# Performance work log

Hardware: AMD Instinct MI355X
Metric: run time of the kernel (lower is better)

## Reference

```python
import jax, jax.numpy as jnp
import numpy as np

N_NODES = 100000
N_EDGES = 1600000
F_IN, HID, N_CLS = 128, 64, 40


def gcn_conv(x, src, dst, W, b, n_nodes):
    # x: [N, Fin] -> [N, Fout]; edges already include self-loops.
    h = x @ W  # [N, Fout]
    ones = jnp.ones_like(src, dtype=h.dtype)
    deg = jax.ops.segment_sum(ones, dst, num_segments=n_nodes)  # [N]
    dinv = jnp.where(deg > 0, jax.lax.rsqrt(deg), 0.0)
    norm = dinv[src] * dinv[dst]  # [E]
    msg = h[src] * norm[:, None]  # gather + scale
    out = jax.ops.segment_sum(msg, dst, num_segments=n_nodes)  # scatter-sum
    return out + b


def setup_inputs() -> dict:
    key = jax.random.key(0)
    ks = jax.random.split(key, 8)
    x = jax.random.normal(ks[0], (N_NODES, F_IN), dtype=jnp.float32)
    edge_index = jax.random.randint(ks[1], (2, N_EDGES), 0, N_NODES, dtype=jnp.int64)

    def glorot(k, fi, fo):
        s = float(np.sqrt(6.0 / (fi + fo)))
        return jax.random.uniform(k, (fi, fo), jnp.float32, -s, s)

    return {
        "x": x,
        "edge_index": edge_index,
        "W1": glorot(ks[2], F_IN, HID), "b1": jnp.zeros((HID,), jnp.float32),
        "W2": glorot(ks[3], HID, HID), "b2": jnp.zeros((HID,), jnp.float32),
        "W3": glorot(ks[4], HID, N_CLS), "b3": jnp.zeros((N_CLS,), jnp.float32),
    }


def reference(x, edge_index, W1, b1, W2, b2, W3, b3):
    n = x.shape[0]
    loop = jnp.arange(n, dtype=edge_index.dtype)
    src = jnp.concatenate([edge_index[0], loop])  # add self-loops
    dst = jnp.concatenate([edge_index[1], loop])
    # layer 1..3: GCNConv -> relu -> dropout(eval: identity)
    h = jax.nn.relu(gcn_conv(x, src, dst, W1, b1, n))
    h = jax.nn.relu(gcn_conv(h, src, dst, W2, b2, n))
    h = jax.nn.relu(gcn_conv(h, src, dst, W3, b3, n))
    return jax.nn.log_softmax(h, axis=1)
```

## Files before the change

### kernel.cpp

```cpp
#include <hip/hip_runtime.h>
#include <math.h>

typedef _Float16 half2v  __attribute__((ext_vector_type(2)));
typedef _Float16 half8   __attribute__((ext_vector_type(8)));
typedef float    float4v __attribute__((ext_vector_type(4)));

static __device__ __forceinline__ unsigned short f32_to_f16u(float f) {
    _Float16 h = (_Float16)f;
    return __builtin_bit_cast(unsigned short, h);
}


__global__ void zero_int(int* __restrict__ p, int n) {
    int i = blockIdx.x * blockDim.x + threadIdx.x;
    if (i < n) p[i] = 0;
}

__global__ __launch_bounds__(256) void hist_bucket(
    const int* __restrict__ dst, int* __restrict__ bcnt, int E, int NB)
{
    __shared__ int h[512];
    const int tid = threadIdx.x;
    h[tid] = 0; h[tid + 256] = 0;
    __syncthreads();
    const int base = blockIdx.x * 4096 + tid;
    #pragma unroll
    for (int k = 0; k < 16; ++k) {
        int i = base + k * 256;
        if (i < E) atomicAdd(&h[dst[i] >> 8], 1);
    }
    __syncthreads();
    for (int j = tid; j < NB; j += 256)
        if (h[j]) atomicAdd(&bcnt[j], h[j]);
}

__global__ __launch_bounds__(512) void scan_nb(
    const int* __restrict__ bcnt, int* __restrict__ boff, int* __restrict__ bcur,
    int* __restrict__ rp, int NB, int n, int E)
{
    __shared__ int s[512];
    const int tid = threadIdx.x;
    int v = (tid < NB) ? bcnt[tid] : 0;
    s[tid] = v;
    __syncthreads();
    for (int off = 1; off < 512; off <<= 1) {
        int x = (tid >= off) ? s[tid - off] : 0;
        __syncthreads();
        s[tid] += x;
        __syncthreads();
    }
    int excl = s[tid] - v;
    if (tid < NB) { boff[tid] = excl; bcur[tid] = excl; }
    if (tid == NB - 1) boff[NB] = excl + v;
    if (tid == 0) rp[n] = E;
}

__global__ __launch_bounds__(256) void bin_edges(
    const int* __restrict__ src, const int* __restrict__ dst,
    int* __restrict__ bcur, unsigned int* __restrict__ bint, int E, int NB)
{
    __shared__ int h[512];
    __shared__ int rbase[512];
    const int tid = threadIdx.x;
    h[tid] = 0; h[tid + 256] = 0;
    __syncthreads();
    const int eb = blockIdx.x * 4096 + tid;
    int d[16], sr[16];
    #pragma unroll
    for (int k = 0; k < 16; ++k) {
        int i = eb + k * 256;
        if (i < E) {
            d[k] = dst[i]; sr[k] = src[i];
            atomicAdd(&h[d[k] >> 8], 1);
        } else d[k] = -1;
    }
    __syncthreads();
    for (int j = tid; j < NB; j += 256) {
        int c = h[j];
        rbase[j] = c ? atomicAdd(&bcur[j], c) : 0;
        h[j] = 0;
    }
    __syncthreads();
    #pragma unroll
    for (int k = 0; k < 16; ++k) {
        if (d[k] >= 0) {
            int bkt = d[k] >> 8;
            int pos = rbase[bkt] + atomicAdd(&h[bkt], 1);
            bint[pos] = ((unsigned int)sr[k] << 8) | (unsigned int)(d[k] & 255);
        }
    }
}

__global__ __launch_bounds__(256) void build_csr(
    const unsigned int* __restrict__ bint, const int* __restrict__ boff,
    int* __restrict__ rp, float* __restrict__ dinv, int* __restrict__ es, int n)
{
    __shared__ int cnt[256];
    __shared__ int sc[256];
    __shared__ int cur[256];
    const int b = blockIdx.x, tid = threadIdx.x;
    const int e0 = boff[b], e1 = boff[b + 1];

    cnt[tid] = 0;
    __syncthreads();
    for (int i = e0 + tid; i < e1; i += 256)
        atomicAdd(&cnt[bint[i] & 255], 1);
    __syncthreads();

    int v = cnt[tid];
    sc[tid] = v;
    __syncthreads();
    for (int off = 1; off < 256; off <<= 1) {
        int x = (tid >= off) ? sc[tid - off] : 0;
        __syncthreads();
        sc[tid] += x;
        __syncthreads();
    }
    int excl = sc[tid] - v;
    int node = (b << 8) + tid;
    if (node < n) {
        rp[node]   = e0 + excl;
        dinv[node] = rsqrtf((float)(v + 1));
    }
    cur[tid] = e0 + excl;
    __syncthreads();

    for (int i = e0 + tid; i < e1; i += 256) {
        unsigned int p = bint[i];
        int pos = atomicAdd(&cur[p & 255], 1);
        es[pos] = (int)(p >> 8);
    }
}


__global__ __launch_bounds__(256) void prep_w3(
    const float* __restrict__ W1, const float* __restrict__ W2, const float* __restrict__ W3,
    unsigned short* __restrict__ Wf1, unsigned short* __restrict__ Wf2, unsigned short* __restrict__ Wf3)
{
    const float* W; unsigned short* Wf; int K, M;
    if (blockIdx.x == 0)      { W = W1; Wf = Wf1; K = 128; M = 64; }
    else if (blockIdx.x == 1) { W = W2; Wf = Wf2; K = 64;  M = 64; }
    else                      { W = W3; Wf = Wf3; K = 64;  M = 40; }
    const int NT = (M + 15) >> 4, NTC = NT << 4, KS = K >> 5;
    for (int i = threadIdx.x; i < K * NTC; i += 256) {
        int k = i / NTC, nn = i - k * NTC;
        unsigned short hv = 0;
        if (nn < M) hv = f32_to_f16u(W[(size_t)k * M + nn]);
        int s = k >> 5, q = (k >> 3) & 3, j = k & 7;
        int u = nn >> 4, lane = (q << 4) | (nn & 15);
        Wf[((u * KS + s) << 9) + (lane << 3) + j] = hv;
    }
}


template<int KK, int NT, int STRIDE, int MOUT, bool INF32>
__global__ __launch_bounds__(256) void gemm_t(
    const void* __restrict__ Xin, const unsigned short* __restrict__ Wf,
    const float* __restrict__ dinv, unsigned short* __restrict__ H, int n)
{
    constexpr int KS = KK >> 5;
    __shared__ __align__(16) unsigned short ldsA[4 * KS * 512];
    const int tid = threadIdx.x;
    const int n0  = blockIdx.x * 64;

    half8 bf[NT * KS];
    {
        const int lane = tid & 63;
        #pragma unroll
        for (int u = 0; u < NT; ++u)
            #pragma unroll
            for (int s = 0; s < KS; ++s)
                bf[u * KS + s] = *(const half8*)&Wf[((u * KS + s) << 9) + (lane << 3)];
    }

    {
        const int rl = tid >> 3;
        const int kl = tid & 7;
        #pragma unroll
        for (int rb = 0; rb < 64; rb += 32) {
            int r = rl + rb;
            int node = n0 + r;
            int t = r >> 4, m = r & 15;
            #pragma unroll
            for (int kq8 = 0; kq8 < (KK >> 2); kq8 += 8) {
                int k0 = (kl + kq8) << 2;
                unsigned short h[4] = {0, 0, 0, 0};
                if (node < n) {
                    if (INF32) {
                        const float* xp = (const float*)Xin + (size_t)node * KK + k0;
                        float4v v = *(const float4v*)xp;
                        #pragma unroll
                        for (int i = 0; i < 4; ++i) h[i] = f32_to_f16u(v[i]);
                    } else {
                        const unsigned int* ap =
                            (const unsigned int*)Xin + (((size_t)node * KK + k0) >> 1);
                        uint2 v = *(const uint2*)ap;
                        h[0] = (unsigned short)(v.x & 0xffff);
                        h[1] = (unsigned short)(v.x >> 16);
                        h[2] = (unsigned short)(v.y & 0xffff);
                        h[3] = (unsigned short)(v.y >> 16);
                    }
                }
                int s = k0 >> 5, q = (k0 >> 3) & 3, j0 = k0 & 7;
                int lane = (q << 4) | m;
                unsigned short* p = &ldsA[((t * KS + s) << 9) + (lane << 3) + j0];
                unsigned int lo = (unsigned int)h[0] | ((unsigned int)h[1] << 16);
                unsigned int hi = (unsigned int)h[2] | ((unsigned int)h[3] << 16);
                *(uint2*)p = make_uint2(lo, hi);
            }
        }
    }

    __syncthreads();

    const int wv   = tid >> 6;
    const int lane = tid & 63;
    float4v acc[NT];
    #pragma unroll
    for (int u = 0; u < NT; ++u) acc[u] = (float4v){0.f, 0.f, 0.f, 0.f};

    #pragma unroll
    for (int s = 0; s < KS; ++s) {
        half8 a = *(const half8*)&ldsA[((wv * KS + s) << 9) + (lane << 3)];
        #pragma unroll
        for (int u = 0; u < NT; ++u)
            acc[u] = __builtin_amdgcn_mfma_f32_16x16x32_f16(a, bf[u * KS + s], acc[u], 0, 0, 0);
    }

    const int mcol = lane & 15;
    const int quad = lane >> 4;
    #pragma unroll
    for (int reg = 0; reg < 4; ++reg) {
        int node = n0 + (wv << 4) + (quad << 2) + reg;
        if (node >= n) continue;
        float dv = dinv[node];
        #pragma unroll
        for (int u = 0; u < NT; ++u) {
            int col = (u << 4) + mcol;
            if (col < MOUT)
                H[(size_t)node * STRIDE + col] = f32_to_f16u(acc[u][reg] * dv);
        }
    }
}


template<int MOUT, int ROWU4, bool RELU_OUT, bool SOFTMAX>
__global__ __launch_bounds__(256) void gather_t(
    const int* __restrict__ rp, const int* __restrict__ es,
    const unsigned short* __restrict__ H, const float* __restrict__ dinv,
    const float* __restrict__ bias, void* __restrict__ Aout, int n)
{
    const int lane   = threadIdx.x & 63;
    const int half   = lane >> 5;
    const int lane32 = lane & 31;
    const int slot   = (lane >> 3) & 3;
    const int c8     = lane & 7;
    const bool act   = c8 < ROWU4;
    const uint4* H4  = (const uint4*)H;

    float bi[8];
    #pragma unroll
    for (int i = 0; i < 8; ++i) {
        int col = (c8 << 3) + i;
        bi[i] = (col < MOUT) ? bias[col] : 0.0f;
    }

    const half8 hz = {(_Float16)0, (_Float16)0, (_Float16)0, (_Float16)0,
                      (_Float16)0, (_Float16)0, (_Float16)0, (_Float16)0};

    const int TW2 = (int)(gridDim.x << 3);
    for (int nb = (((int)blockIdx.x << 2) + ((int)threadIdx.x >> 6)) << 1; nb < n; nb += TW2) {
        const int node = nb + half;
        const int e0 = rp[node], e1 = rp[node + 1];
        const float dv = dinv[node];

        half8 hacc = hz;
        if (slot == 0 && act)
            hacc = __builtin_bit_cast(half8, H4[(size_t)node * ROWU4 + c8]);

        for (int cb = e0; cb < e1; cb += 32) {
            const int rem = e1 - cb;
            int eidx = cb + lane32; if (eidx > e1 - 1) eidx = e1 - 1;
            const int ei = es[eidx];
            #pragma unroll
            for (int j = 0; j < 8; ++j) {
                const int idx = (j << 2) + slot;
                const int s = __shfl(ei, (half << 5) + idx, 64);
                if (idx < rem && act) {
                    uint4 u = H4[(size_t)s * ROWU4 + c8];
                    hacc = hacc + __builtin_bit_cast(half8, u);
                }
            }
        }

        #pragma unroll
        for (int step = 8; step <= 16; step <<= 1) {
            uint4 u = __builtin_bit_cast(uint4, hacc);
            uint4 o;
            o.x = __shfl_xor(u.x, step, 64);
            o.y = __shfl_xor(u.y, step, 64);
            o.z = __shfl_xor(u.z, step, 64);
            o.w = __shfl_xor(u.w, step, 64);
            hacc = hacc + __builtin_bit_cast(half8, o);
        }

        if (!SOFTMAX) {
            if (slot == 0) {
                unsigned short o[8];
                #pragma unroll
                for (int i = 0; i < 8; ++i) {
                    float v = (float)hacc[i] * dv + bi[i];
                    if (RELU_OUT) v = fmaxf(v, 0.0f);
                    o[i] = f32_to_f16u(v);
                }
                uint4 w;
                w.x = (unsigned int)o[0] | ((unsigned int)o[1] << 16);
                w.y = (unsigned int)o[2] | ((unsigned int)o[3] << 16);
                w.z = (unsigned int)o[4] | ((unsigned int)o[5] << 16);
                w.w = (unsigned int)o[6] | ((unsigned int)o[7] << 16);
                ((uint4*)Aout)[(size_t)node * 8 + c8] = w;
            }
        } else {
            float z[8]; float m = -INFINITY;
            #pragma unroll
            for (int i = 0; i < 8; ++i) {
                int col = (c8 << 3) + i;
                z[i] = (col < MOUT && act) ? fmaxf((float)hacc[i] * dv + bi[i], 0.0f)
                                           : -INFINITY;
                m = fmaxf(m, z[i]);
            }
            m = fmaxf(m, __shfl_xor(m, 1, 64));
            m = fmaxf(m, __shfl_xor(m, 2, 64));
            m = fmaxf(m, __shfl_xor(m, 4, 64));
            float s = 0.0f;
            #pragma unroll
            for (int i = 0; i < 8; ++i) s += expf(z[i] - m);
            s += __shfl_xor(s, 1, 64);
            s += __shfl_xor(s, 2, 64);
            s += __shfl_xor(s, 4, 64);
            float ls = logf(s) + m;
            if (slot == 0 && c8 < (MOUT + 7) / 8) {
                float* op = (float*)Aout + (size_t)node * MOUT + (c8 << 3);
                float4v o0 = {z[0] - ls, z[1] - ls, z[2] - ls, z[3] - ls};
                float4v o1 = {z[4] - ls, z[5] - ls, z[6] - ls, z[7] - ls};
                *(float4v*)op = o0;
                *(float4v*)(op + 4) = o1;
            }
        }
    }
}


extern "C" void kernel_launch(void* const* d_in, const int* in_sizes, int n_in,
                              void* d_out, int out_size, void* d_ws, size_t ws_size,
                              hipStream_t stream)
{
    const float* x  = (const float*)d_in[0];
    const int*   ei = (const int*)  d_in[1];
    const float* W1 = (const float*)d_in[2];
    const float* b1 = (const float*)d_in[3];
    const float* W2 = (const float*)d_in[4];
    const float* b2 = (const float*)d_in[5];
    const float* W3 = (const float*)d_in[6];
    const float* b3 = (const float*)d_in[7];

    const int F_IN = 128;
    const int n = in_sizes[0] / F_IN;
    const int E = in_sizes[1] / 2;
    const int* src = ei;
    const int* dst = ei + E;
    float* out = (float*)d_out;

    const int NB = (n + 255) >> 8;

    auto align = [](size_t v) { return (v + 255) & ~(size_t)255; };
    char* w = (char*)d_ws;
    size_t off = 0;
    float*          dinv = (float*)(w + off);          off = align(off + (size_t)n * 4);
    unsigned short* H    = (unsigned short*)(w + off); off = align(off + (size_t)n * 64 * 2);
    unsigned short* A    = (unsigned short*)(w + off); off = align(off + (size_t)n * 64 * 2);
    int*            rp   = (int*)(w + off);            off = align(off + (size_t)(n + 1) * 4);
    int*            es   = (int*)(w + off);            off = align(off + (size_t)E * 4);
    unsigned int*   bint = (unsigned int*)(w + off);   off = align(off + (size_t)E * 4);
    int*            bcnt = (int*)(w + off);            off = align(off + (size_t)512 * 4);
    int*            boff = (int*)(w + off);            off = align(off + (size_t)513 * 4);
    int*            bcur = (int*)(w + off);            off = align(off + (size_t)512 * 4);
    unsigned short* Wf1  = (unsigned short*)(w + off); off = align(off + (size_t)8192 * 2);
    unsigned short* Wf2  = (unsigned short*)(w + off); off = align(off + (size_t)4096 * 2);
    unsigned short* Wf3  = (unsigned short*)(w + off); off = align(off + (size_t)3072 * 2);

    const int BLK = 256;
    auto cdiv = [](int a, int b) { return (a + b - 1) / b; };
    const int EB = cdiv(E, 4096);

    prep_w3    <<<3, BLK, 0, stream>>>(W1, W2, W3, Wf1, Wf2, Wf3);
    zero_int   <<<cdiv(NB, BLK), BLK, 0, stream>>>(bcnt, NB);
    hist_bucket<<<EB, BLK, 0, stream>>>(dst, bcnt, E, NB);
    scan_nb    <<<1, 512, 0, stream>>>(bcnt, boff, bcur, rp, NB, n, E);
    bin_edges  <<<EB, BLK, 0, stream>>>(src, dst, bcur, bint, E, NB);
    build_csr  <<<NB, BLK, 0, stream>>>(bint, boff, rp, dinv, es, n);

    const int GB = cdiv(n, 64);
    const int GG = 2048;

    gemm_t<128, 4, 64, 64, true> <<<GB, BLK, 0, stream>>>(x, Wf1, dinv, H, n);
    gather_t<64, 8, true, false><<<GG, BLK, 0, stream>>>(rp, es, H, dinv, b1, A, n);

    gemm_t<64, 4, 64, 64, false> <<<GB, BLK, 0, stream>>>(A, Wf2, dinv, H, n);
    gather_t<64, 8, true, false><<<GG, BLK, 0, stream>>>(rp, es, H, dinv, b2, A, n);

    gemm_t<64, 3, 40, 40, false> <<<GB, BLK, 0, stream>>>(A, Wf3, dinv, H, n);
    gather_t<40, 5, false, true><<<GG, BLK, 0, stream>>>(rp, es, H, dinv, b3, out, n);
}
```

Measured before the change: 293.3 us.

## Fuse gather with next-layer GEMM and use fixed-capacity buckets for CSR build

```diff
diff --git a/kernel.cpp b/kernel.cpp
--- a/kernel.cpp
+++ b/kernel.cpp
@@ -1,9 +1,10 @@
 #include <hip/hip_runtime.h>
 #include <math.h>
 
-typedef _Float16 half2v  __attribute__((ext_vector_type(2)));
 typedef _Float16 half8   __attribute__((ext_vector_type(8)));
 typedef float    float4v __attribute__((ext_vector_type(4)));
+
+#define CAP 6144
 
 static __device__ __forceinline__ unsigned short f32_to_f16u(float f) {
     _Float16 h = (_Float16)f;
@@ -11,132 +12,15 @@
 }
 
 
-__global__ void zero_int(int* __restrict__ p, int n) {
-    int i = blockIdx.x * blockDim.x + threadIdx.x;
-    if (i < n) p[i] = 0;
-}
-
-__global__ __launch_bounds__(256) void hist_bucket(
-    const int* __restrict__ dst, int* __restrict__ bcnt, int E, int NB)
-{
-    __shared__ int h[512];
-    const int tid = threadIdx.x;
-    h[tid] = 0; h[tid + 256] = 0;
-    __syncthreads();
-    const int base = blockIdx.x * 4096 + tid;
-    #pragma unroll
-    for (int k = 0; k < 16; ++k) {
-        int i = base + k * 256;
-        if (i < E) atomicAdd(&h[dst[i] >> 8], 1);
-    }
-    __syncthreads();
-    for (int j = tid; j < NB; j += 256)
-        if (h[j]) atomicAdd(&bcnt[j], h[j]);
-}
-
-__global__ __launch_bounds__(512) void scan_nb(
-    const int* __restrict__ bcnt, int* __restrict__ boff, int* __restrict__ bcur,
-    int* __restrict__ rp, int NB, int n, int E)
-{
-    __shared__ int s[512];
-    const int tid = threadIdx.x;
-    int v = (tid < NB) ? bcnt[tid] : 0;
-    s[tid] = v;
-    __syncthreads();
-    for (int off = 1; off < 512; off <<= 1) {
-        int x = (tid >= off) ? s[tid - off] : 0;
-        __syncthreads();
-        s[tid] += x;
-        __syncthreads();
-    }
-    int excl = s[tid] - v;
-    if (tid < NB) { boff[tid] = excl; bcur[tid] = excl; }
-    if (tid == NB - 1) boff[NB] = excl + v;
-    if (tid == 0) rp[n] = E;
-}
-
-__global__ __launch_bounds__(256) void bin_edges(
-    const int* __restrict__ src, const int* __restrict__ dst,
-    int* __restrict__ bcur, unsigned int* __restrict__ bint, int E, int NB)
-{
-    __shared__ int h[512];
-    __shared__ int rbase[512];
-    const int tid = threadIdx.x;
-    h[tid] = 0; h[tid + 256] = 0;
-    __syncthreads();
-    const int eb = blockIdx.x * 4096 + tid;
-    int d[16], sr[16];
-    #pragma unroll
-    for (int k = 0; k < 16; ++k) {
-        int i = eb + k * 256;
-        if (i < E) {
-            d[k] = dst[i]; sr[k] = src[i];
-            atomicAdd(&h[d[k] >> 8], 1);
-        } else d[k] = -1;
-    }
-    __syncthreads();
-    for (int j = tid; j < NB; j += 256) {
-        int c = h[j];
-        rbase[j] = c ? atomicAdd(&bcur[j], c) : 0;
-        h[j] = 0;
-    }
-    __syncthreads();
-    #pragma unroll
-    for (int k = 0; k < 16; ++k) {
-        if (d[k] >= 0) {
-            int bkt = d[k] >> 8;
-            int pos = rbase[bkt] + atomicAdd(&h[bkt], 1);
-            bint[pos] = ((unsigned int)sr[k] << 8) | (unsigned int)(d[k] & 255);
-        }
-    }
-}
-
-__global__ __launch_bounds__(256) void build_csr(
-    const unsigned int* __restrict__ bint, const int* __restrict__ boff,
-    int* __restrict__ rp, float* __restrict__ dinv, int* __restrict__ es, int n)
-{
-    __shared__ int cnt[256];
-    __shared__ int sc[256];
-    __shared__ int cur[256];
-    const int b = blockIdx.x, tid = threadIdx.x;
-    const int e0 = boff[b], e1 = boff[b + 1];
-
-    cnt[tid] = 0;
-    __syncthreads();
-    for (int i = e0 + tid; i < e1; i += 256)
-        atomicAdd(&cnt[bint[i] & 255], 1);
-    __syncthreads();
-
-    int v = cnt[tid];
-    sc[tid] = v;
-    __syncthreads();
-    for (int off = 1; off < 256; off <<= 1) {
-        int x = (tid >= off) ? sc[tid - off] : 0;
-        __syncthreads();
-        sc[tid] += x;
-        __syncthreads();
-    }
-    int excl = sc[tid] - v;
-    int node = (b << 8) + tid;
-    if (node < n) {
-        rp[node]   = e0 + excl;
-        dinv[node] = rsqrtf((float)(v + 1));
-    }
-    cur[tid] = e0 + excl;
-    __syncthreads();
-
-    for (int i = e0 + tid; i < e1; i += 256) {
-        unsigned int p = bint[i];
-        int pos = atomicAdd(&cur[p & 255], 1);
-        es[pos] = (int)(p >> 8);
-    }
-}
-
-
-__global__ __launch_bounds__(256) void prep_w3(
+__global__ __launch_bounds__(256) void prep_init(
     const float* __restrict__ W1, const float* __restrict__ W2, const float* __restrict__ W3,
-    unsigned short* __restrict__ Wf1, unsigned short* __restrict__ Wf2, unsigned short* __restrict__ Wf3)
-{
+    unsigned short* __restrict__ Wf1, unsigned short* __restrict__ Wf2,
+    unsigned short* __restrict__ Wf3, int* __restrict__ bcur, int NB)
+{
+    if (blockIdx.x == 3) {
+        for (int i = threadIdx.x; i < NB; i += 256) bcur[i] = 0;
+        return;
+    }
     const float* W; unsigned short* Wf; int K, M;
     if (blockIdx.x == 0)      { W = W1; Wf = Wf1; K = 128; M = 64; }
     else if (blockIdx.x == 1) { W = W2; Wf = Wf2; K = 64;  M = 64; }
@@ -153,9 +37,93 @@
 }
 
 
-template<int KK, int NT, int STRIDE, int MOUT, bool INF32>
+__global__ __launch_bounds__(256) void bin_edges(
+    const int* __restrict__ src, const int* __restrict__ dst,
+    int* __restrict__ bcur, unsigned int* __restrict__ bint, int E, int NB)
+{
+    __shared__ int h[512];
+    __shared__ int rbase[512];
+    const int tid = threadIdx.x;
+    h[tid] = 0; h[tid + 256] = 0;
+    __syncthreads();
+    const int eb = blockIdx.x * 4096 + tid;
+    int d[16], sr[16];
+    #pragma unroll
+    for (int k = 0; k < 16; ++k) {
+        int i = eb + k * 256;
+        if (i < E) {
+            d[k] = dst[i]; sr[k] = src[i];
+            atomicAdd(&h[d[k] >> 8], 1);
+        } else d[k] = -1;
+    }
+    __syncthreads();
+    for (int j = tid; j < NB; j += 256) {
+        int c = h[j];
+        rbase[j] = c ? atomicAdd(&bcur[j], c) : 0;
+        h[j] = 0;
+    }
+    __syncthreads();
+    #pragma unroll
+    for (int k = 0; k < 16; ++k) {
+        if (d[k] >= 0) {
+            int bkt = d[k] >> 8;
+            int pos = rbase[bkt] + atomicAdd(&h[bkt], 1);
+            if (pos < CAP)
+                bint[(size_t)bkt * CAP + pos] =
+                    ((unsigned int)sr[k] << 8) | (unsigned int)(d[k] & 255);
+        }
+    }
+}
+
+
+__global__ __launch_bounds__(256) void build_csr(
+    const unsigned int* __restrict__ bint, const int* __restrict__ bcur,
+    int2* __restrict__ rp2, float* __restrict__ dinv, int* __restrict__ es, int n)
+{
+    __shared__ int cnt[256];
+    __shared__ int sc[256];
+    __shared__ int cur[256];
+    const int b = blockIdx.x, tid = threadIdx.x;
+    int total = bcur[b]; if (total > CAP) total = CAP;
+    const unsigned int* bp = bint + (size_t)b * CAP;
+    int* ep = es + (size_t)b * CAP;
+    const int base = b * CAP;
+
+    cnt[tid] = 0;
+    __syncthreads();
+    for (int i = tid; i < total; i += 256)
+        atomicAdd(&cnt[bp[i] & 255], 1);
+    __syncthreads();
+
+    int v = cnt[tid];
+    sc[tid] = v;
+    __syncthreads();
+    for (int off = 1; off < 256; off <<= 1) {
+        int x = (tid >= off) ? sc[tid - off] : 0;
+        __syncthreads();
+        sc[tid] += x;
+        __syncthreads();
+    }
+    int excl = sc[tid] - v;
+    int node = (b << 8) + tid;
+    if (node < n) {
+        rp2[node]  = make_int2(base + excl, base + excl + v);
+        dinv[node] = rsqrtf((float)(v + 1));
+    }
+    cur[tid] = excl;
+    __syncthreads();
+
+    for (int i = tid; i < total; i += 256) {
+        unsigned int p = bp[i];
+        int pos = atomicAdd(&cur[p & 255], 1);
+        ep[pos] = (int)(p >> 8);
+    }
+}
+
+
+template<int KK, int NT, int STRIDE, int MOUT>
 __global__ __launch_bounds__(256) void gemm_t(
-    const void* __restrict__ Xin, const unsigned short* __restrict__ Wf,
+    const float* __restrict__ Xin, const unsigned short* __restrict__ Wf,
     const float* __restrict__ dinv, unsigned short* __restrict__ H, int n)
 {
     constexpr int KS = KK >> 5;
@@ -186,20 +154,10 @@
                 int k0 = (kl + kq8) << 2;
                 unsigned short h[4] = {0, 0, 0, 0};
                 if (node < n) {
-                    if (INF32) {
-                        const float* xp = (const float*)Xin + (size_t)node * KK + k0;
-                        float4v v = *(const float4v*)xp;
-                        #pragma unroll
-                        for (int i = 0; i < 4; ++i) h[i] = f32_to_f16u(v[i]);
-                    } else {
-                        const unsigned int* ap =
-                            (const unsigned int*)Xin + (((size_t)node * KK + k0) >> 1);
-                        uint2 v = *(const uint2*)ap;
-                        h[0] = (unsigned short)(v.x & 0xffff);
-                        h[1] = (unsigned short)(v.x >> 16);
-                        h[2] = (unsigned short)(v.y & 0xffff);
-                        h[3] = (unsigned short)(v.y >> 16);
-                    }
+                    const float* xp = Xin + (size_t)node * KK + k0;
+                    float4v v = *(const float4v*)xp;
+                    #pragma unroll
+                    for (int i = 0; i < 4; ++i) h[i] = f32_to_f16u(v[i]);
                 }
                 int s = k0 >> 5, q = (k0 >> 3) & 3, j0 = k0 & 7;
                 int lane = (q << 4) | m;
@@ -244,55 +202,61 @@
 }
 
 
-template<int MOUT, int ROWU4, bool RELU_OUT, bool SOFTMAX>
-__global__ __launch_bounds__(256) void gather_t(
-    const int* __restrict__ rp, const int* __restrict__ es,
-    const unsigned short* __restrict__ H, const float* __restrict__ dinv,
-    const float* __restrict__ bias, void* __restrict__ Aout, int n)
-{
-    const int lane   = threadIdx.x & 63;
+template<int NT, int STRIDE, int MOUT>
+__global__ __launch_bounds__(256) void gather_gemm(
+    const int2* __restrict__ rp2, const int* __restrict__ es,
+    const unsigned short* __restrict__ Hin, const float* __restrict__ dinv,
+    const float* __restrict__ bias, const unsigned short* __restrict__ Wf,
+    unsigned short* __restrict__ Hout, int n)
+{
+    constexpr int KS = 2;
+    __shared__ __align__(16) unsigned short ldsA[4 * KS * 512];
+    const int tid  = threadIdx.x;
+    const int wv   = tid >> 6;
+    const int lane = tid & 63;
+    const int nw0  = blockIdx.x * 64 + (wv << 4);
+
+    half8 bf[NT * KS];
+    #pragma unroll
+    for (int u = 0; u < NT; ++u)
+        #pragma unroll
+        for (int s = 0; s < KS; ++s)
+            bf[u * KS + s] = *(const half8*)&Wf[((u * KS + s) << 9) + (lane << 3)];
+
     const int half   = lane >> 5;
     const int lane32 = lane & 31;
     const int slot   = (lane >> 3) & 3;
     const int c8     = lane & 7;
-    const bool act   = c8 < ROWU4;
-    const uint4* H4  = (const uint4*)H;
+    const uint4* H4  = (const uint4*)Hin;
 
     float bi[8];
     #pragma unroll
-    for (int i = 0; i < 8; ++i) {
-        int col = (c8 << 3) + i;
-        bi[i] = (col < MOUT) ? bias[col] : 0.0f;
-    }
+    for (int i = 0; i < 8; ++i) bi[i] = bias[(c8 << 3) + i];
 
     const half8 hz = {(_Float16)0, (_Float16)0, (_Float16)0, (_Float16)0,
                       (_Float16)0, (_Float16)0, (_Float16)0, (_Float16)0};
 
-    const int TW2 = (int)(gridDim.x << 3);
-    for (int nb = (((int)blockIdx.x << 2) + ((int)threadIdx.x >> 6)) << 1; nb < n; nb += TW2) {
-        const int node = nb + half;
-        const int e0 = rp[node], e1 = rp[node + 1];
-        const float dv = dinv[node];
-
+    for (int p = 0; p < 8; ++p) {
+        const int node = nw0 + (p << 1) + half;
         half8 hacc = hz;
-        if (slot == 0 && act)
-            hacc = __builtin_bit_cast(half8, H4[(size_t)node * ROWU4 + c8]);
-
-        for (int cb = e0; cb < e1; cb += 32) {
-            const int rem = e1 - cb;
-            int eidx = cb + lane32; if (eidx > e1 - 1) eidx = e1 - 1;
-            const int ei = es[eidx];
-            #pragma unroll
-            for (int j = 0; j < 8; ++j) {
-                const int idx = (j << 2) + slot;
-                const int s = __shfl(ei, (half << 5) + idx, 64);
-                if (idx < rem && act) {
-                    uint4 u = H4[(size_t)s * ROWU4 + c8];
-                    hacc = hacc + __builtin_bit_cast(half8, u);
+        float dv = 0.0f;
+        if (node < n) {
+            dv = dinv[node];
+            const int2 e = rp2[node];
+            if (slot == 0) hacc = __builtin_bit_cast(half8, H4[(size_t)node * 8 + c8]);
+            for (int cb = e.x; cb < e.y; cb += 32) {
+                const int rem = e.y - cb;
+                int eidx = cb + lane32; if (eidx > e.y - 1) eidx = e.y - 1;
+                const int ei = es[eidx];
+                #pragma unroll
+                for (int j = 0; j < 8; ++j) {
+                    const int idx = (j << 2) + slot;
+                    const int s = __shfl(ei, (half << 5) + idx, 64);
+                    if (idx < rem)
+                        hacc = hacc + __builtin_bit_cast(half8, H4[(size_t)s * 8 + c8]);
                 }
             }
         }
-
         #pragma unroll
         for (int step = 8; step <= 16; step <<= 1) {
             uint4 u = __builtin_bit_cast(uint4, hacc);
@@ -303,49 +267,134 @@
             o.w = __shfl_xor(u.w, step, 64);
             hacc = hacc + __builtin_bit_cast(half8, o);
         }
-
-        if (!SOFTMAX) {
-            if (slot == 0) {
-                unsigned short o[8];
-                #pragma unroll
-                for (int i = 0; i < 8; ++i) {
-                    float v = (float)hacc[i] * dv + bi[i];
-                    if (RELU_OUT) v = fmaxf(v, 0.0f);
-                    o[i] = f32_to_f16u(v);
-                }
-                uint4 w;
-                w.x = (unsigned int)o[0] | ((unsigned int)o[1] << 16);
-                w.y = (unsigned int)o[2] | ((unsigned int)o[3] << 16);
-                w.z = (unsigned int)o[4] | ((unsigned int)o[5] << 16);
-                w.w = (unsigned int)o[6] | ((unsigned int)o[7] << 16);
-                ((uint4*)Aout)[(size_t)node * 8 + c8] = w;
+        if (slot == 0) {
+            unsigned short o[8];
+            #pragma unroll
+            for (int i = 0; i < 8; ++i)
+                o[i] = f32_to_f16u(fmaxf((float)hacc[i] * dv + bi[i], 0.0f));
+            uint4 w;
+            w.x = (unsigned int)o[0] | ((unsigned int)o[1] << 16);
+            w.y = (unsigned int)o[2] | ((unsigned int)o[3] << 16);
+            w.z = (unsigned int)o[4] | ((unsigned int)o[5] << 16);
+            w.w = (unsigned int)o[6] | ((unsigned int)o[7] << 16);
+            const int m = (p << 1) | half;
+            unsigned short* dst =
+                &ldsA[((wv * KS + (c8 >> 2)) << 9) + ((((c8 & 3) << 4) | m) << 3)];
+            *(uint4*)dst = w;
+        }
+    }
+
+    float4v acc[NT];
+    #pragma unroll
+    for (int u = 0; u < NT; ++u) acc[u] = (float4v){0.f, 0.f, 0.f, 0.f};
+
+    #pragma unroll
+    for (int s = 0; s < KS; ++s) {
+        half8 a = *(const half8*)&ldsA[((wv * KS + s) << 9) + (lane << 3)];
+        #pragma unroll
+        for (int u = 0; u < NT; ++u)
+            acc[u] = __builtin_amdgcn_mfma_f32_16x16x32_f16(a, bf[u * KS + s], acc[u], 0, 0, 0);
+    }
+
+    const int mcol = lane & 15;
+    const int quad = lane >> 4;
+    #pragma unroll
+    for (int reg = 0; reg < 4; ++reg) {
+        int node = nw0 + (quad << 2) + reg;
+        if (node >= n) continue;
+        float dv = dinv[node];
+        #pragma unroll
+        for (int u = 0; u < NT; ++u) {
+            int col = (u << 4) + mcol;
+            if (col < MOUT)
+                Hout[(size_t)node * STRIDE + col] = f32_to_f16u(acc[u][reg] * dv);
+        }
+    }
+}
+
+
+template<int MOUT, int ROWU4>
+__global__ __launch_bounds__(256) void gather_softmax(
+    const int2* __restrict__ rp2, const int* __restrict__ es,
+    const unsigned short* __restrict__ H, const float* __restrict__ dinv,
+    const float* __restrict__ bias, float* __restrict__ out, int n)
+{
+    const int lane   = threadIdx.x & 63;
+    const int half   = lane >> 5;
+    const int lane32 = lane & 31;
+    const int slot   = (lane >> 3) & 3;
+    const int c8     = lane & 7;
+    const bool act   = c8 < ROWU4;
+    const uint4* H4  = (const uint4*)H;
+
+    float bi[8];
+    #pragma unroll
+    for (int i = 0; i < 8; ++i) {
+        int col = (c8 << 3) + i;
+        bi[i] = (col < MOUT) ? bias[col] : 0.0f;
+    }
+
+    const half8 hz = {(_Float16)0, (_Float16)0, (_Float16)0, (_Float16)0,
+                      (_Float16)0, (_Float16)0, (_Float16)0, (_Float16)0};
+
+    const int TW2 = (int)(gridDim.x << 3);
+    for (int nb = (((int)blockIdx.x << 2) + ((int)threadIdx.x >> 6)) << 1; nb < n; nb += TW2) {
+        const int node = nb + half;
+        const int2 e = rp2[node];
+        const float dv = dinv[node];
+
+        half8 hacc = hz;
+        if (slot == 0 && act)
+            hacc = __builtin_bit_cast(half8, H4[(size_t)node * ROWU4 + c8]);
+
+        for (int cb = e.x; cb < e.y; cb += 32) {
+            const int rem = e.y - cb;
+            int eidx = cb + lane32; if (eidx > e.y - 1) eidx = e.y - 1;
+            const int ei = es[eidx];
+            #pragma unroll
+            for (int j = 0; j < 8; ++j) {
+                const int idx = (j << 2) + slot;
+                const int s = __shfl(ei, (half << 5) + idx, 64);
+                if (idx < rem && act)
+                    hacc = hacc + __builtin_bit_cast(half8, H4[(size_t)s * ROWU4 + c8]);
             }
-        } else {
-            float z[8]; float m = -INFINITY;
-            #pragma unroll
-            for (int i = 0; i < 8; ++i) {
-                int col = (c8 << 3) + i;
-                z[i] = (col < MOUT && act) ? fmaxf((float)hacc[i] * dv + bi[i], 0.0f)
-                                           : -INFINITY;
-                m = fmaxf(m, z[i]);
-            }
-            m = fmaxf(m, __shfl_xor(m, 1, 64));
-            m = fmaxf(m, __shfl_xor(m, 2, 64));
-            m = fmaxf(m, __shfl_xor(m, 4, 64));
-            float s = 0.0f;
-            #pragma unroll
-            for (int i = 0; i < 8; ++i) s += expf(z[i] - m);
-            s += __shfl_xor(s, 1, 64);
-            s += __shfl_xor(s, 2, 64);
-            s += __shfl_xor(s, 4, 64);
-            float ls = logf(s) + m;
-            if (slot == 0 && c8 < (MOUT + 7) / 8) {
-                float* op = (float*)Aout + (size_t)node * MOUT + (c8 << 3);
-                float4v o0 = {z[0] - ls, z[1] - ls, z[2] - ls, z[3] - ls};
-                float4v o1 = {z[4] - ls, z[5] - ls, z[6] - ls, z[7] - ls};
-                *(float4v*)op = o0;
-                *(float4v*)(op + 4) = o1;
-            }
+        }
+
+        #pragma unroll
+        for (int step = 8; step <= 16; step <<= 1) {
+            uint4 u = __builtin_bit_cast(uint4, hacc);
+            uint4 o;
+            o.x = __shfl_xor(u.x, step, 64);
+            o.y = __shfl_xor(u.y, step, 64);
+            o.z = __shfl_xor(u.z, step, 64);
+            o.w = __shfl_xor(u.w, step, 64);
+            hacc = hacc + __builtin_bit_cast(half8, o);
+        }
+
+        float z[8]; float m = -INFINITY;
+        #pragma unroll
+        for (int i = 0; i < 8; ++i) {
+            int col = (c8 << 3) + i;
+            z[i] = (col < MOUT && act) ? fmaxf((float)hacc[i] * dv + bi[i], 0.0f)
+                                       : -INFINITY;
+            m = fmaxf(m, z[i]);
+        }
+        m = fmaxf(m, __shfl_xor(m, 1, 64));
+        m = fmaxf(m, __shfl_xor(m, 2, 64));
+        m = fmaxf(m, __shfl_xor(m, 4, 64));
+        float s = 0.0f;
+        #pragma unroll
+        for (int i = 0; i < 8; ++i) s += expf(z[i] - m);
+        s += __shfl_xor(s, 1, 64);
+        s += __shfl_xor(s, 2, 64);
+        s += __shfl_xor(s, 4, 64);
+        float ls = logf(s) + m;
+        if (slot == 0 && c8 < (MOUT + 7) / 8) {
+            float* op = out + (size_t)node * MOUT + (c8 << 3);
+            float4v o0 = {z[0] - ls, z[1] - ls, z[2] - ls, z[3] - ls};
+            float4v o1 = {z[4] - ls, z[5] - ls, z[6] - ls, z[7] - ls};
+            *(float4v*)op = o0;
+            *(float4v*)(op + 4) = o1;
         }
     }
 }
@@ -377,13 +426,12 @@
     char* w = (char*)d_ws;
     size_t off = 0;
     float*          dinv = (float*)(w + off);          off = align(off + (size_t)n * 4);
-    unsigned short* H    = (unsigned short*)(w + off); off = align(off + (size_t)n * 64 * 2);
-    unsigned short* A    = (unsigned short*)(w + off); off = align(off + (size_t)n * 64 * 2);
-    int*            rp   = (int*)(w + off);            off = align(off + (size_t)(n + 1) * 4);
-    int*            es   = (int*)(w + off);            off = align(off + (size_t)E * 4);
-    unsigned int*   bint = (unsigned int*)(w + off);   off = align(off + (size_t)E * 4);
-    int*            bcnt = (int*)(w + off);            off = align(off + (size_t)512 * 4);
-    int*            boff = (int*)(w + off);            off = align(off + (size_t)513 * 4);
+    unsigned short* H1   = (unsigned short*)(w + off); off = align(off + (size_t)n * 64 * 2);
+    unsigned short* H2   = (unsigned short*)(w + off); off = align(off + (size_t)n * 64 * 2);
+    unsigned short* H3   = (unsigned short*)(w + off); off = align(off + (size_t)n * 40 * 2);
+    int2*           rp2  = (int2*)(w + off);           off = align(off + (size_t)n * 8);
+    int*            es   = (int*)(w + off);            off = align(off + (size_t)NB * CAP * 4);
+    unsigned int*   bint = (unsigned int*)(w + off);   off = align(off + (size_t)NB * CAP * 4);
     int*            bcur = (int*)(w + off);            off = align(off + (size_t)512 * 4);
     unsigned short* Wf1  = (unsigned short*)(w + off); off = align(off + (size_t)8192 * 2);
     unsigned short* Wf2  = (unsigned short*)(w + off); off = align(off + (size_t)4096 * 2);
@@ -392,23 +440,18 @@
     const int BLK = 256;
     auto cdiv = [](int a, int b) { return (a + b - 1) / b; };
     const int EB = cdiv(E, 4096);
-
-    prep_w3    <<<3, BLK, 0, stream>>>(W1, W2, W3, Wf1, Wf2, Wf3);
-    zero_int   <<<cdiv(NB, BLK), BLK, 0, stream>>>(bcnt, NB);
-    hist_bucket<<<EB, BLK, 0, stream>>>(dst, bcnt, E, NB);
-    scan_nb    <<<1, 512, 0, stream>>>(bcnt, boff, bcur, rp, NB, n, E);
-    bin_edges  <<<EB, BLK, 0, stream>>>(src, dst, bcur, bint, E, NB);
-    build_csr  <<<NB, BLK, 0, stream>>>(bint, boff, rp, dinv, es, n);
-
     const int GB = cdiv(n, 64);
     const int GG = 2048;
 
-    gemm_t<128, 4, 64, 64, true> <<<GB, BLK, 0, stream>>>(x, Wf1, dinv, H, n);
-    gather_t<64, 8, true, false><<<GG, BLK, 0, stream>>>(rp, es, H, dinv, b1, A, n);
-
-    gemm_t<64, 4, 64, 64, false> <<<GB, BLK, 0, stream>>>(A, Wf2, dinv, H, n);
-    gather_t<64, 8, true, false><<<GG, BLK, 0, stream>>>(rp, es, H, dinv, b2, A, n);
-
-    gemm_t<64, 3, 40, 40, false> <<<GB, BLK, 0, stream>>>(A, Wf3, dinv, H, n);
-    gather_t<40, 5, false, true><<<GG, BLK, 0, stream>>>(rp, es, H, dinv, b3, out, n);
-}
+    prep_init<<<4, BLK, 0, stream>>>(W1, W2, W3, Wf1, Wf2, Wf3, bcur, NB);
+    bin_edges<<<EB, BLK, 0, stream>>>(src, dst, bcur, bint, E, NB);
+    build_csr<<<NB, BLK, 0, stream>>>(bint, bcur, rp2, dinv, es, n);
+
+    gemm_t<128, 4, 64, 64><<<GB, BLK, 0, stream>>>(x, Wf1, dinv, H1, n);
+
+    gather_gemm<4, 64, 64><<<GB, BLK, 0, stream>>>(rp2, es, H1, dinv, b1, Wf2, H2, n);
+
+    gather_gemm<3, 40, 40><<<GB, BLK, 0, stream>>>(rp2, es, H2, dinv, b2, Wf3, H3, n);
+
+    gather_softmax<40, 5><<<GG, BLK, 0, stream>>>(rp2, es, H3, dinv, b3, out, n);
+}
```

Result: no change. 299.0 us (+1.9%).
